# Kernel tuning notes

Measured on AMD Instinct MI355X. Metric: run time of the kernel, lower is better.

## Reference

```python
import jax, jax.numpy as jnp
import numpy as np
from jax import lax

# Config mirroring __init__ defaults
TEMP = 0.1           # temperature (constant schedule; set_epoch never called)
KSIZE = 11           # dilation_kernel_size
MAX_POS = 2048       # max_pos_per_image
NEG_RATIO = 5.0      # neg_pos_ratio
EPS = 1e-8
KN = int(NEG_RATIO * MAX_POS)   # max negatives per image (10240)
KC = 2 * KN                      # rim candidate pool for hard mining (20480)


def _forward(features, labels):
    B, C, H, W = features.shape
    HW = H * W
    fg = labels > 0                                   # (B,H,W)
    # Dilate foreground via max-pool (kernel KSIZE, stride 1, SAME) -> rim band
    dil = lax.reduce_window(fg.astype(jnp.float32), -jnp.inf, lax.max,
                            (1, KSIZE, KSIZE), (1, 1, 1), 'SAME') > 0
    rim = dil & (~fg)
    # L2-normalized per-pixel features, (B,HW,C)
    f = features.reshape(B, C, HW).transpose(0, 2, 1)
    f = f / jnp.maximum(jnp.linalg.norm(f, axis=-1, keepdims=True), EPS)
    fg_flat = fg.reshape(B, HW)
    rim_flat = rim.reshape(B, HW)
    rank = jnp.arange(HW, dtype=jnp.float32) / HW     # deterministic tiebreak

    def per_image(fi, fgi, rimi):
        # --- sample positives (deterministic raster-order selection of fg pixels) ---
        _, pidx = lax.top_k(fgi.astype(jnp.float32) * 2.0 - rank, MAX_POS)
        vp = fgi[pidx]                                # valid-positive mask (P,)
        pf = fi[pidx]                                 # (P,C)
        # --- rim candidate pool ---
        _, cidx = lax.top_k(rimi.astype(jnp.float32) * 2.0 - rank, KC)
        vc = rimi[cidx]
        cf = fi[cidx]                                 # (KC,C)
        # --- hard negative mining: negatives most similar to any positive ---
        sim = pf @ cf.T                               # (P,KC)
        max_sim = jnp.max(jnp.where(vp[:, None], sim, -jnp.inf), axis=0)
        nvals, nsel = lax.top_k(jnp.where(vc, max_sim, -jnp.inf), KN)
        n_allowed = jnp.minimum(jnp.floor(NEG_RATIO * jnp.sum(vp)), KN)
        vn = jnp.isfinite(nvals) & (jnp.arange(KN) < n_allowed)
        nf = cf[nsel]                                 # (KN,C)
        # --- contrastive loss: positives attract, rim negatives repel ---
        lpp = (pf @ pf.T) / TEMP                      # (P,P)
        lpn = (pf @ nf.T) / TEMP                      # (P,KN)
        eye = jnp.eye(MAX_POS, dtype=bool)
        mpp = vp[:, None] & vp[None, :] & (~eye)
        mpn = vp[:, None] & vn[None, :]
        NEGC = jnp.float32(-1e30)
        all_logits = jnp.concatenate([jnp.where(mpp, lpp, NEGC),
                                      jnp.where(mpn, lpn, NEGC)], axis=1)
        denom = jax.nn.logsumexp(all_logits, axis=1)  # (P,)
        npairs = jnp.sum(mpp, axis=1)
        li = -jnp.sum(jnp.where(mpp, lpp - denom[:, None], 0.0), axis=1) \
             / jnp.maximum(npairs, 1)
        av = vp & (npairs > 0)
        img_loss = jnp.sum(jnp.where(av, li, 0.0)) / jnp.maximum(jnp.sum(av), 1)
        return img_loss, jnp.any(av)

    losses, has = jax.vmap(per_image)(f, fg_flat, rim_flat)
    return jnp.sum(jnp.where(has, losses, 0.0)) / jnp.maximum(jnp.sum(has), 1)


def setup_inputs() -> dict:
    key = jax.random.key(0)
    k1, k2 = jax.random.split(key)
    features = jax.random.normal(k1, (4, 64, 384, 384), dtype=jnp.float32)
    labels = jax.random.randint(k2, (4, 384, 384), 0, 2).astype(jnp.int64)
    return {"features": features, "labels": labels}


def reference(features, labels):
    return _forward(features, labels)
```

## Files before the change

### kernel.cpp

```cpp
#include <hip/hip_runtime.h>
#include <hip/hip_bf16.h>

#define DEVI __device__ __forceinline__

static constexpr int cB = 4, cC = 64, cH = 384, cW = 384;
static constexpr int cHW = cH * cW;
static constexpr int cP  = 2048;
static constexpr int cKC = 20480;
static constexpr int cKN = 10240;
static constexpr int cNT = cP + cKN;
static constexpr float cTEMP_INV = 10.0f;
static constexpr int cCHUNK = 2048;
static constexpr int cNB = cHW / cCHUNK;
static constexpr int cNCH = 8;
static constexpr int cTPC = (cNT / 16) / cNCH;

using f32x4  = __attribute__((ext_vector_type(4))) float;
using bf16x8 = __attribute__((ext_vector_type(8))) __bf16;

static constexpr size_t off_fg   = 0;
static constexpr size_t off_tmp  = off_fg   + (size_t)cB * cHW;
static constexpr size_t off_rim  = off_tmp  + (size_t)cB * cHW;
static constexpr size_t off_pidx = off_rim  + (size_t)cB * cHW;
static constexpr size_t off_cidx = off_pidx + (size_t)cB * cP * 4;
static constexpr size_t off_scal = off_cidx + (size_t)cB * cKC * 4;
static constexpr size_t off_EL   = off_scal + 256;
static constexpr size_t off_msim = off_EL   + (size_t)cB * cP * 8;
static constexpr size_t off_nsel = off_msim + (size_t)cB * 2 * cKC * 4;
static constexpr size_t off_G    = off_nsel + (size_t)cB * cKN * 4;
static constexpr size_t off_cf   = off_G    + (size_t)cB * cNT * cC * 2;
static constexpr size_t off_bcnt = off_cf   + (size_t)cB * cKC * cC * 2;
static constexpr size_t off_boff = off_bcnt + (size_t)cB * cNB * 4;

__global__ void k_fg(const int* labels, unsigned char* fg) {
  int i = blockIdx.x * 256 + threadIdx.x;
  if (i < cB * cHW) fg[i] = labels[i] > 0;
}

__global__ void k_hdil(const unsigned char* fg, unsigned char* tmp) {
  int i = blockIdx.x * 256 + threadIdx.x;
  if (i >= cB * cHW) return;
  int x = i % cW;
  int rowbase = i - x;
  int lo = max(x - 5, 0), hi = min(x + 5, cW - 1);
  unsigned char m = 0;
  for (int xx = lo; xx <= hi; xx++) m |= fg[rowbase + xx];
  tmp[i] = m;
}

__global__ __launch_bounds__(256) void k_vdil_count(const unsigned char* tmp, const unsigned char* fg,
                                                    unsigned char* rim, int* blkcnt) {
  __shared__ int red[256];
  int b = blockIdx.y, blk = blockIdx.x, tid = threadIdx.x;
  int base = blk * cCHUNK + tid * 8;
  const unsigned char* tb  = tmp + (size_t)b * cHW;
  const unsigned char* fgb = fg  + (size_t)b * cHW;
  unsigned long long fv = *(const unsigned long long*)(fgb + base);
  unsigned long long pk = 0;
  int crim = 0;
#pragma unroll
  for (int e = 0; e < 8; e++) {
    int p = base + e;
    int y = p / cW, x = p - y * cW;
    int lo = max(y - 5, 0), hi = min(y + 5, cH - 1);
    unsigned char m = 0;
    for (int yy = lo; yy <= hi; yy++) m |= tb[yy * cW + x];
    unsigned char f = (unsigned char)((fv >> (8 * e)) & 1);
    unsigned char rv = m & (f ^ 1);
    pk |= (unsigned long long)rv << (8 * e);
    crim += rv;
  }
  *(unsigned long long*)(rim + (size_t)b * cHW + base) = pk;
  int cfg = __popcll(fv & 0x0101010101010101ULL);
  red[tid] = cfg | (crim << 16);
  __syncthreads();
  for (int s = 128; s > 0; s >>= 1) {
    if (tid < s) red[tid] += red[tid + s];
    __syncthreads();
  }
  if (tid == 0) blkcnt[b * cNB + blk] = red[0];
}

__global__ __launch_bounds__(128) void k_offsets(const int* blkcnt, int2* blkoff, int* scal) {
  __shared__ int sf[128], sr[128];
  int b = blockIdx.x, tid = threadIdx.x;
  int v = (tid < cNB) ? blkcnt[b * cNB + tid] : 0;
  int f = v & 0xffff, r = v >> 16;
  sf[tid] = f; sr[tid] = r;
  __syncthreads();
  for (int d = 1; d < 128; d <<= 1) {
    int tf = (tid >= d) ? sf[tid - d] : 0;
    int tr = (tid >= d) ? sr[tid - d] : 0;
    __syncthreads();
    sf[tid] += tf; sr[tid] += tr;
    __syncthreads();
  }
  if (tid < cNB) blkoff[b * cNB + tid] = make_int2(sf[tid] - f, sr[tid] - r);
  if (tid == 0) {
    int nfg = sf[cNB - 1], nrim = sr[cNB - 1];
    scal[b * 16 + 0] = nfg;
    scal[b * 16 + 1] = min(nfg, cP);
    scal[b * 16 + 2] = min(nrim, cKC);
    scal[b * 16 + 4] = nrim;
  }
}

__device__ int scan_excl_256(int v, int* lds) {
  int tid = threadIdx.x;
  lds[tid] = v;
  __syncthreads();
  for (int d = 1; d < 256; d <<= 1) {
    int t = (tid >= d) ? lds[tid - d] : 0;
    __syncthreads();
    lds[tid] += t;
    __syncthreads();
  }
  int e = lds[tid] - v;
  __syncthreads();
  return e;
}

__global__ __launch_bounds__(256) void k_scatter(const unsigned char* fg, const unsigned char* rim,
                                                 const int2* blkoff, const int* scal,
                                                 int* pidx, int* cidx) {
  __shared__ int lds[256];
  int b = blockIdx.y, blk = blockIdx.x, tid = threadIdx.x;
  int2 off = blkoff[b * cNB + blk];
  int nfg  = scal[b * 16 + 0];
  int nrim = scal[b * 16 + 4];
  bool needf = (off.x < cP)  || (nfg  < cP);
  bool needr = (off.y < cKC) || (nrim < cKC);
  if (!needf && !needr) return;
  int base = blk * cCHUNK + tid * 8;
  const unsigned char* fgb  = fg  + (size_t)b * cHW;
  const unsigned char* rimb = rim + (size_t)b * cHW;
  unsigned long long fv = *(const unsigned long long*)(fgb + base);
  unsigned long long rv = *(const unsigned long long*)(rimb + base);
  int cfg  = __popcll(fv & 0x0101010101010101ULL);
  int crim = __popcll(rv & 0x0101010101010101ULL);
  int ex = scan_excl_256(cfg | (crim << 16), lds);
  int of  = off.x + (ex & 0xffff);
  int orr = off.y + (ex >> 16);
  int* pout = pidx + (size_t)b * cP;
  int* cout = cidx + (size_t)b * cKC;
#pragma unroll
  for (int e = 0; e < 8; e++) {
    int p = base + e;
    int f = (int)((fv >> (8 * e)) & 1);
    int r = (int)((rv >> (8 * e)) & 1);
    if (f) { if (of < cP) pout[of] = p; of++; }
    else if (nfg < cP) { int o = nfg + (p - of); if (o < cP) pout[o] = p; }
    if (r) { if (orr < cKC) cout[orr] = p; orr++; }
    else if (nrim < cKC) { int o = nrim + (p - orr); if (o < cKC) cout[o] = p; }
  }
}

__global__ __launch_bounds__(256) void k_gather_norm(const float* feat, const int* idxs, int idx_stride,
                                                     int count, __hip_bfloat16* dst, size_t dst_img_stride) {
  int b = blockIdx.y;
  int i = blockIdx.x * 256 + threadIdx.x;
  if (i >= count) return;
  int p = idxs[(size_t)b * idx_stride + i];
  const float* fb = feat + (size_t)b * cC * cHW + p;
  float v[cC];
  float ss = 0.f;
#pragma unroll
  for (int c = 0; c < cC; c++) { float t = fb[(size_t)c * cHW]; v[c] = t; ss += t * t; }
  float sc = 1.0f / fmaxf(sqrtf(ss), 1e-8f);
  __hip_bfloat16* out = dst + (size_t)b * dst_img_stride + (size_t)i * cC;
#pragma unroll
  for (int c = 0; c < cC; c++) out[c] = __float2bfloat16(v[c] * sc);
}

__global__ __launch_bounds__(256) void k_mine(const __hip_bfloat16* G, const __hip_bfloat16* cf,
                                              const int* scal, float* msim) {
  int b = blockIdx.z, rc = blockIdx.y;
  int P_valid = scal[b * 16 + 1];
  int wave = threadIdx.x >> 6, lane = threadIdx.x & 63;
  int lr = lane & 15, quad = lane >> 4;
  int colbase = blockIdx.x * 128 + wave * 32;
  float* msout = msim + ((size_t)b * 2 + rc) * cKC;
  int mt0 = rc * (cP / 32);
  int chunk_lo = mt0 * 16;
  if (chunk_lo >= P_valid) {
    if (quad == 0) {
      msout[colbase + lr]      = -INFINITY;
      msout[colbase + 16 + lr] = -INFINITY;
    }
    return;
  }
  bool chunk_full = (chunk_lo + cP / 2) <= P_valid;
  const __bf16* pf  = (const __bf16*)(G  + (size_t)b * cNT * cC);
  const __bf16* cfb = (const __bf16*)(cf + (size_t)b * cKC * cC);

  bf16x8 bfr[2][2];
#pragma unroll
  for (int t = 0; t < 2; t++) {
    const __bf16* src = cfb + (size_t)(colbase + t * 16 + lr) * cC + quad * 8;
    bfr[t][0] = *(const bf16x8*)src;
    bfr[t][1] = *(const bf16x8*)(src + 32);
  }
  float cmax0 = -INFINITY, cmax1 = -INFINITY;
#pragma unroll 2
  for (int mt = mt0; mt < mt0 + cP / 32; mt++) {
    const __bf16* asrc = pf + (size_t)(mt * 16 + lr) * cC + quad * 8;
    bf16x8 a0 = *(const bf16x8*)asrc;
    bf16x8 a1 = *(const bf16x8*)(asrc + 32);
    f32x4 acc0 = {0, 0, 0, 0}, acc1 = {0, 0, 0, 0};
    acc0 = __builtin_amdgcn_mfma_f32_16x16x32_bf16(a0, bfr[0][0], acc0, 0, 0, 0);
    acc0 = __builtin_amdgcn_mfma_f32_16x16x32_bf16(a1, bfr[0][1], acc0, 0, 0, 0);
    acc1 = __builtin_amdgcn_mfma_f32_16x16x32_bf16(a0, bfr[1][0], acc1, 0, 0, 0);
    acc1 = __builtin_amdgcn_mfma_f32_16x16x32_bf16(a1, bfr[1][1], acc1, 0, 0, 0);
    if (chunk_full) {
#pragma unroll
      for (int r = 0; r < 4; r++) {
        cmax0 = fmaxf(cmax0, acc0[r]);
        cmax1 = fmaxf(cmax1, acc1[r]);
      }
    } else {
      int rb = mt * 16 + quad * 4;
#pragma unroll
      for (int r = 0; r < 4; r++) {
        bool rv = (rb + r) < P_valid;
        cmax0 = fmaxf(cmax0, rv ? acc0[r] : -INFINITY);
        cmax1 = fmaxf(cmax1, rv ? acc1[r] : -INFINITY);
      }
    }
  }
  cmax0 = fmaxf(cmax0, __shfl_xor(cmax0, 16));
  cmax0 = fmaxf(cmax0, __shfl_xor(cmax0, 32));
  cmax1 = fmaxf(cmax1, __shfl_xor(cmax1, 16));
  cmax1 = fmaxf(cmax1, __shfl_xor(cmax1, 32));
  if (quad == 0) {
    msout[colbase + lr]      = cmax0;
    msout[colbase + 16 + lr] = cmax1;
  }
}

DEVI unsigned f2key(float f) {
  unsigned u = __float_as_uint(f);
  return (u & 0x80000000u) ? ~u : (u | 0x80000000u);
}

__device__ int scan_excl_1024(int v, int* lds, int* total) {
  int tid = threadIdx.x;
  lds[tid] = v;
  __syncthreads();
  for (int d = 1; d < 1024; d <<= 1) {
    int t = (tid >= d) ? lds[tid - d] : 0;
    __syncthreads();
    lds[tid] += t;
    __syncthreads();
  }
  *total = lds[1023];
  int e = lds[tid] - v;
  __syncthreads();
  return e;
}

__global__ __launch_bounds__(1024) void k_selneg(const float* msim, int* nsel, int* scal) {
  __shared__ int hist[256];
  __shared__ int suf[256];
  __shared__ int lds[1024];
  __shared__ unsigned sh_prefix;
  __shared__ int sh_rem;
  int b = blockIdx.x, tid = threadIdx.x;
  const float* ms0 = msim + ((size_t)b * 2 + 0) * cKC;
  const float* ms1 = msim + ((size_t)b * 2 + 1) * cKC;
  int P_valid = scal[b * 16 + 1], C_valid = scal[b * 16 + 2];
  int n_allowed = min(5 * P_valid, cKN);
  int nfin = (P_valid > 0) ? C_valid : 0;
  int KEEP = min(n_allowed, nfin);
  if (tid == 0) scal[b * 16 + 3] = KEEP;
  if (KEEP == 0) return;

  unsigned prefix = 0;
  int remaining = KEEP;
  for (int shift = 24; shift >= 0; shift -= 8) {
    if (tid < 256) hist[tid] = 0;
    __syncthreads();
    for (int c = tid; c < cKC; c += 1024) {
      unsigned key = (c < C_valid) ? f2key(fmaxf(ms0[c], ms1[c])) : 0u;
      if (shift == 24 || (key >> (shift + 8)) == prefix)
        atomicAdd(&hist[(key >> shift) & 255], 1);
    }
    __syncthreads();
    if (tid < 256) suf[tid] = hist[tid];
    __syncthreads();
    for (int d = 1; d < 256; d <<= 1) {
      int t = (tid < 256 && tid + d < 256) ? suf[tid + d] : 0;
      __syncthreads();
      if (tid < 256) suf[tid] += t;
      __syncthreads();
    }
    if (tid < 256) {
      int s = suf[tid];
      int sn = (tid < 255) ? suf[tid + 1] : 0;
      if (s >= remaining && sn < remaining) {
        sh_prefix = (prefix << 8) | (unsigned)tid;
        sh_rem = remaining - sn;
      }
    }
    __syncthreads();
    prefix = sh_prefix; remaining = sh_rem;
    __syncthreads();
  }
  unsigned T = prefix;

  const int CH2 = cKC / 1024;
  int s = tid * CH2;
  unsigned keys[CH2];
  int cntA = 0, cntT = 0;
  for (int e = 0; e < CH2; e++) {
    int c = s + e;
    unsigned key = (c < C_valid) ? f2key(fmaxf(ms0[c], ms1[c])) : 0u;
    keys[e] = key;
    cntA += (key > T);
    cntT += (key == T);
  }
  int totA, totT;
  int offA = scan_excl_1024(cntA, lds, &totA);
  int offT = scan_excl_1024(cntT, lds, &totT);
  int* out = nsel + (size_t)b * cKN;
  int oa = offA, ot = offT;
  for (int e = 0; e < CH2; e++) {
    unsigned key = keys[e];
    if (key > T) { out[oa++] = s + e; }
    else if (key == T) { if (ot < remaining) out[totA + ot] = s + e; ot++; }
  }
}

__global__ __launch_bounds__(256) void k_gather_neg(const __hip_bfloat16* cf, const int* nsel,
                                                    const int* scal, __hip_bfloat16* G) {
  int b = blockIdx.y;
  int KEEP = scal[b * 16 + 3];
  int t = blockIdx.x * 256 + threadIdx.x;
  int k = t >> 3, part = t & 7;
  if (k >= cKN) return;
  int4 val = {0, 0, 0, 0};
  if (k < KEEP) {
    int src = nsel[(size_t)b * cKN + k];
    val = *(const int4*)((const __bf16*)(cf + (size_t)b * cKC * cC) + (size_t)src * cC + part * 8);
  }
  *(int4*)((__bf16*)(G + (size_t)b * cNT * cC) + (size_t)(cP + k) * cC + part * 8) = val;
}

__global__ __launch_bounds__(256) void k_loss_part(const __hip_bfloat16* G, const int* scal, float2* EL) {
  __shared__ float sE[4][32];
  __shared__ float sL[4][32];
  int b = blockIdx.z;
  int P_valid = scal[b * 16 + 1];
  int KEEP = scal[b * 16 + 3];
  int wave = threadIdx.x >> 6, lane = threadIdx.x & 63;
  int lr = lane & 15, quad = lane >> 4;
  int rowbase = blockIdx.x * 32;
  const __bf16* Gb = (const __bf16*)G + (size_t)b * cNT * cC;

  bf16x8 afr[2][2];
#pragma unroll
  for (int rt = 0; rt < 2; rt++) {
    const __bf16* src = Gb + (size_t)(rowbase + rt * 16 + lr) * cC + quad * 8;
    afr[rt][0] = *(const bf16x8*)src;
    afr[rt][1] = *(const bf16x8*)(src + 32);
  }
  float eacc[2][4] = {{0, 0, 0, 0}, {0, 0, 0, 0}};
  float lacc[2][4] = {{0, 0, 0, 0}, {0, 0, 0, 0}};
  int ct0 = blockIdx.y * cTPC;
  for (int ct = ct0 + wave; ct < ct0 + cTPC; ct += 4) {
    int tb = ct * 16;
    bool is_pos = tb < cP;
    int vlimit = is_pos ? P_valid : (cP + KEEP);
    if (tb >= vlimit) continue;
    bool all_valid = (tb + 16) <= vlimit;
    bool has_diag = is_pos && (tb >= rowbase) && (tb < rowbase + 32);
    const __bf16* bsrc = Gb + (size_t)(tb + lr) * cC + quad * 8;
    bf16x8 b0 = *(const bf16x8*)bsrc;
    bf16x8 b1 = *(const bf16x8*)(bsrc + 32);
    f32x4 acc[2];
#pragma unroll
    for (int rt = 0; rt < 2; rt++) {
      f32x4 a = {0, 0, 0, 0};
      a = __builtin_amdgcn_mfma_f32_16x16x32_bf16(afr[rt][0], b0, a, 0, 0, 0);
      a = __builtin_amdgcn_mfma_f32_16x16x32_bf16(afr[rt][1], b1, a, 0, 0, 0);
      acc[rt] = a;
    }
    if (all_valid && !has_diag) {
      if (is_pos) {
#pragma unroll
        for (int rt = 0; rt < 2; rt++)
#pragma unroll
          for (int r = 0; r < 4; r++) {
            float logit = acc[rt][r] * cTEMP_INV;
            eacc[rt][r] += __expf(logit);
            lacc[rt][r] += logit;
          }
      } else {
#pragma unroll
        for (int rt = 0; rt < 2; rt++)
#pragma unroll
          for (int r = 0; r < 4; r++)
            eacc[rt][r] += __expf(acc[rt][r] * cTEMP_INV);
      }
    } else {
      bool colv = (tb + lr) < vlimit;
#pragma unroll
      for (int rt = 0; rt < 2; rt++) {
        int rb = rowbase + rt * 16 + quad * 4;
#pragma unroll
        for (int r = 0; r < 4; r++) {
          float logit = acc[rt][r] * cTEMP_INV;
          bool use = colv && !(has_diag && (tb + lr) == (rb + r));
          float e = __expf(logit);
          eacc[rt][r] += use ? e : 0.0f;
          if (is_pos) lacc[rt][r] += use ? logit : 0.0f;
        }
      }
    }
  }
#pragma unroll
  for (int rt = 0; rt < 2; rt++) {
#pragma unroll
    for (int r = 0; r < 4; r++) {
      float e = eacc[rt][r], l = lacc[rt][r];
#pragma unroll
      for (int d = 1; d < 16; d <<= 1) {
        e += __shfl_xor(e, d);
        l += __shfl_xor(l, d);
      }
      if (lr == 0) {
        sE[wave][rt * 16 + quad * 4 + r] = e;
        sL[wave][rt * 16 + quad * 4 + r] = l;
      }
    }
  }
  __syncthreads();
  if (threadIdx.x < 32) {
    int row = rowbase + threadIdx.x;
    float E = sE[0][threadIdx.x] + sE[1][threadIdx.x] + sE[2][threadIdx.x] + sE[3][threadIdx.x];
    float L = sL[0][threadIdx.x] + sL[1][threadIdx.x] + sL[2][threadIdx.x] + sL[3][threadIdx.x];
    atomicAdd(&EL[(size_t)b * cP + row].x, E);
    atomicAdd(&EL[(size_t)b * cP + row].y, L);
  }
}

__global__ __launch_bounds__(1024) void k_loss_fin(const int* scal, const float2* EL, float* out) {
  __shared__ float ssum[16];
  int tid = threadIdx.x;
  int b = tid >> 8, t = tid & 255;
  int Pv = scal[b * 16 + 1];
  float s = 0.f;
  if (Pv >= 2) {
    float inv = 1.0f / (float)(Pv - 1);
#pragma unroll
    for (int e = 0; e < 8; e++) {
      int row = t * 8 + e;
      if (row < Pv) {
        float2 el = EL[(size_t)b * cP + row];
        s += logf(el.x) - el.y * inv;
      }
    }
  }
#pragma unroll
  for (int d = 1; d < 64; d <<= 1) s += __shfl_xor(s, d);
  if ((tid & 63) == 0) ssum[tid >> 6] = s;
  __syncthreads();
  if (tid == 0) {
    float tot = 0.f;
    int cnt = 0;
    for (int bb = 0; bb < cB; bb++) {
      int P = scal[bb * 16 + 1];
      if (P >= 2) {
        float is = ssum[bb * 4] + ssum[bb * 4 + 1] + ssum[bb * 4 + 2] + ssum[bb * 4 + 3];
        tot += is / (float)P;
        cnt++;
      }
    }
    out[0] = tot / (float)(cnt > 0 ? cnt : 1);
  }
}

extern "C" void kernel_launch(void* const* d_in, const int* in_sizes, int n_in,
                              void* d_out, int out_size, void* d_ws, size_t ws_size,
                              hipStream_t stream) {
  const float* feat = (const float*)d_in[0];
  const int* labels = (const int*)d_in[1];
  char* ws = (char*)d_ws;
  unsigned char* fg  = (unsigned char*)(ws + off_fg);
  unsigned char* tmp = (unsigned char*)(ws + off_tmp);
  unsigned char* rim = (unsigned char*)(ws + off_rim);
  int* pidx = (int*)(ws + off_pidx);
  int* cidx = (int*)(ws + off_cidx);
  int* scal = (int*)(ws + off_scal);
  float2* EL = (float2*)(ws + off_EL);
  float* msim = (float*)(ws + off_msim);
  int* nsel = (int*)(ws + off_nsel);
  __hip_bfloat16* G  = (__hip_bfloat16*)(ws + off_G);
  __hip_bfloat16* cf = (__hip_bfloat16*)(ws + off_cf);
  int* blkcnt = (int*)(ws + off_bcnt);
  int2* blkoff = (int2*)(ws + off_boff);
  float* out = (float*)d_out;

  int nElem = cB * cHW;
  hipMemsetAsync(EL, 0, (size_t)cB * cP * 8, stream);
  k_fg<<<(nElem + 255) / 256, 256, 0, stream>>>(labels, fg);
  k_hdil<<<(nElem + 255) / 256, 256, 0, stream>>>(fg, tmp);
  k_vdil_count<<<dim3(cNB, cB), 256, 0, stream>>>(tmp, fg, rim, blkcnt);
  k_offsets<<<cB, 128, 0, stream>>>(blkcnt, blkoff, scal);
  k_scatter<<<dim3(cNB, cB), 256, 0, stream>>>(fg, rim, blkoff, scal, pidx, cidx);
  k_gather_norm<<<dim3(cP / 256, cB), 256, 0, stream>>>(feat, pidx, cP, cP, G, (size_t)cNT * cC);
  k_gather_norm<<<dim3(cKC / 256, cB), 256, 0, stream>>>(feat, cidx, cKC, cKC, cf, (size_t)cKC * cC);
  k_mine<<<dim3(cKC / 128, 2, cB), 256, 0, stream>>>(G, cf, scal, msim);
  k_selneg<<<cB, 1024, 0, stream>>>(msim, nsel, scal);
  k_gather_neg<<<dim3(cKN * 8 / 256, cB), 256, 0, stream>>>(cf, nsel, scal, G);
  k_loss_part<<<dim3(cP / 32, cNCH, cB), 256, 0, stream>>>(G, scal, EL);
  k_loss_fin<<<1, 1024, 0, stream>>>(scal, EL, out);
}
```

Baseline: 416.9 us.

## Fuse preprocessing kernels, widen mining and loss tiles, drop atomics

Merges the fg threshold and horizontal dilation into one bit-packed kernel and vectorizes the vertical dilation over 8-byte words. Merges the two gather-normalize launches into one. Widens k_mine to 128 columns per wave with A-fragment prefetch, and k_loss_part to 64 rows per block. Per-chunk partial sums replace atomics and the memset, and the final kernel reduces them. These cut launch count, redundant loads and atomic traffic, at the cost of more register pressure and fewer blocks in the mining and loss kernels.

```diff
diff --git a/kernel.cpp b/kernel.cpp
--- a/kernel.cpp
+++ b/kernel.cpp
@@ -25,27 +25,37 @@
 static constexpr size_t off_cidx = off_pidx + (size_t)cB * cP * 4;
 static constexpr size_t off_scal = off_cidx + (size_t)cB * cKC * 4;
 static constexpr size_t off_EL   = off_scal + 256;
-static constexpr size_t off_msim = off_EL   + (size_t)cB * cP * 8;
+static constexpr size_t off_msim = off_EL   + (size_t)cNCH * cB * cP * 8;
 static constexpr size_t off_nsel = off_msim + (size_t)cB * 2 * cKC * 4;
 static constexpr size_t off_G    = off_nsel + (size_t)cB * cKN * 4;
 static constexpr size_t off_cf   = off_G    + (size_t)cB * cNT * cC * 2;
 static constexpr size_t off_bcnt = off_cf   + (size_t)cB * cKC * cC * 2;
 static constexpr size_t off_boff = off_bcnt + (size_t)cB * cNB * 4;
 
-__global__ void k_fg(const int* labels, unsigned char* fg) {
-  int i = blockIdx.x * 256 + threadIdx.x;
-  if (i < cB * cHW) fg[i] = labels[i] > 0;
-}
-
-__global__ void k_hdil(const unsigned char* fg, unsigned char* tmp) {
-  int i = blockIdx.x * 256 + threadIdx.x;
-  if (i >= cB * cHW) return;
-  int x = i % cW;
-  int rowbase = i - x;
-  int lo = max(x - 5, 0), hi = min(x + 5, cW - 1);
-  unsigned char m = 0;
-  for (int xx = lo; xx <= hi; xx++) m |= fg[rowbase + xx];
-  tmp[i] = m;
+DEVI f32x4 mfma16(bf16x8 a, bf16x8 b, f32x4 c) {
+  return __builtin_amdgcn_mfma_f32_16x16x32_bf16(a, b, c, 0, 0, 0);
+}
+
+__global__ __launch_bounds__(256) void k_fg_hdil(const int* labels, unsigned char* fg, unsigned char* tmp) {
+  int t = blockIdx.x * 256 + threadIdx.x;
+  int base = t * 8;
+  int x0 = base % cW;
+  const int* lb = labels + (base - x0);
+  unsigned m = 0;
+#pragma unroll
+  for (int j = 0; j < 18; j++) {
+    int x = x0 - 5 + j;
+    int v = (x >= 0 && x < cW) ? (lb[x] > 0) : 0;
+    m |= (unsigned)v << j;
+  }
+  unsigned long long fgb = 0, tmb = 0;
+#pragma unroll
+  for (int e = 0; e < 8; e++) {
+    fgb |= (unsigned long long)((m >> (e + 5)) & 1u) << (8 * e);
+    tmb |= (unsigned long long)(((m >> e) & 0x7FFu) ? 1u : 0u) << (8 * e);
+  }
+  *(unsigned long long*)(fg + base)  = fgb;
+  *(unsigned long long*)(tmp + base) = tmb;
 }
 
 __global__ __launch_bounds__(256) void k_vdil_count(const unsigned char* tmp, const unsigned char* fg,
@@ -56,22 +66,14 @@
   const unsigned char* tb  = tmp + (size_t)b * cHW;
   const unsigned char* fgb = fg  + (size_t)b * cHW;
   unsigned long long fv = *(const unsigned long long*)(fgb + base);
-  unsigned long long pk = 0;
-  int crim = 0;
-#pragma unroll
-  for (int e = 0; e < 8; e++) {
-    int p = base + e;
-    int y = p / cW, x = p - y * cW;
-    int lo = max(y - 5, 0), hi = min(y + 5, cH - 1);
-    unsigned char m = 0;
-    for (int yy = lo; yy <= hi; yy++) m |= tb[yy * cW + x];
-    unsigned char f = (unsigned char)((fv >> (8 * e)) & 1);
-    unsigned char rv = m & (f ^ 1);
-    pk |= (unsigned long long)rv << (8 * e);
-    crim += rv;
-  }
+  int y = base / cW, x = base % cW;
+  int lo = max(y - 5, 0), hi = min(y + 5, cH - 1);
+  unsigned long long m8 = 0;
+  for (int yy = lo; yy <= hi; yy++) m8 |= *(const unsigned long long*)(tb + yy * cW + x);
+  unsigned long long pk = m8 & (fv ^ 0x0101010101010101ULL);
   *(unsigned long long*)(rim + (size_t)b * cHW + base) = pk;
-  int cfg = __popcll(fv & 0x0101010101010101ULL);
+  int cfg  = __popcll(fv & 0x0101010101010101ULL);
+  int crim = __popcll(pk & 0x0101010101010101ULL);
   red[tid] = cfg | (crim << 16);
   __syncthreads();
   for (int s = 128; s > 0; s >>= 1) {
@@ -155,19 +157,27 @@
   }
 }
 
-__global__ __launch_bounds__(256) void k_gather_norm(const float* feat, const int* idxs, int idx_stride,
-                                                     int count, __hip_bfloat16* dst, size_t dst_img_stride) {
+__global__ __launch_bounds__(256) void k_gather_norm(const float* feat, const int* pidx, const int* cidx,
+                                                     __hip_bfloat16* G, __hip_bfloat16* cf) {
   int b = blockIdx.y;
-  int i = blockIdx.x * 256 + threadIdx.x;
-  if (i >= count) return;
-  int p = idxs[(size_t)b * idx_stride + i];
+  int bx = blockIdx.x;
+  int p;
+  __hip_bfloat16* out;
+  if (bx < cP / 256) {
+    int i = bx * 256 + threadIdx.x;
+    p = pidx[(size_t)b * cP + i];
+    out = G + (size_t)b * cNT * cC + (size_t)i * cC;
+  } else {
+    int i = (bx - cP / 256) * 256 + threadIdx.x;
+    p = cidx[(size_t)b * cKC + i];
+    out = cf + (size_t)b * cKC * cC + (size_t)i * cC;
+  }
   const float* fb = feat + (size_t)b * cC * cHW + p;
   float v[cC];
   float ss = 0.f;
 #pragma unroll
   for (int c = 0; c < cC; c++) { float t = fb[(size_t)c * cHW]; v[c] = t; ss += t * t; }
   float sc = 1.0f / fmaxf(sqrtf(ss), 1e-8f);
-  __hip_bfloat16* out = dst + (size_t)b * dst_img_stride + (size_t)i * cC;
 #pragma unroll
   for (int c = 0; c < cC; c++) out[c] = __float2bfloat16(v[c] * sc);
 }
@@ -178,62 +188,66 @@
   int P_valid = scal[b * 16 + 1];
   int wave = threadIdx.x >> 6, lane = threadIdx.x & 63;
   int lr = lane & 15, quad = lane >> 4;
-  int colbase = blockIdx.x * 128 + wave * 32;
+  int colbase = (blockIdx.x * 4 + wave) * 128;
   float* msout = msim + ((size_t)b * 2 + rc) * cKC;
-  int mt0 = rc * (cP / 32);
+  int mt0 = rc * 64;
   int chunk_lo = mt0 * 16;
   if (chunk_lo >= P_valid) {
     if (quad == 0) {
-      msout[colbase + lr]      = -INFINITY;
-      msout[colbase + 16 + lr] = -INFINITY;
+#pragma unroll
+      for (int tt = 0; tt < 8; tt++) msout[colbase + tt * 16 + lr] = -INFINITY;
     }
     return;
   }
-  bool chunk_full = (chunk_lo + cP / 2) <= P_valid;
+  bool chunk_full = (chunk_lo + 1024) <= P_valid;
   const __bf16* pf  = (const __bf16*)(G  + (size_t)b * cNT * cC);
   const __bf16* cfb = (const __bf16*)(cf + (size_t)b * cKC * cC);
 
-  bf16x8 bfr[2][2];
-#pragma unroll
-  for (int t = 0; t < 2; t++) {
-    const __bf16* src = cfb + (size_t)(colbase + t * 16 + lr) * cC + quad * 8;
-    bfr[t][0] = *(const bf16x8*)src;
-    bfr[t][1] = *(const bf16x8*)(src + 32);
-  }
-  float cmax0 = -INFINITY, cmax1 = -INFINITY;
-#pragma unroll 2
-  for (int mt = mt0; mt < mt0 + cP / 32; mt++) {
-    const __bf16* asrc = pf + (size_t)(mt * 16 + lr) * cC + quad * 8;
-    bf16x8 a0 = *(const bf16x8*)asrc;
-    bf16x8 a1 = *(const bf16x8*)(asrc + 32);
-    f32x4 acc0 = {0, 0, 0, 0}, acc1 = {0, 0, 0, 0};
-    acc0 = __builtin_amdgcn_mfma_f32_16x16x32_bf16(a0, bfr[0][0], acc0, 0, 0, 0);
-    acc0 = __builtin_amdgcn_mfma_f32_16x16x32_bf16(a1, bfr[0][1], acc0, 0, 0, 0);
-    acc1 = __builtin_amdgcn_mfma_f32_16x16x32_bf16(a0, bfr[1][0], acc1, 0, 0, 0);
-    acc1 = __builtin_amdgcn_mfma_f32_16x16x32_bf16(a1, bfr[1][1], acc1, 0, 0, 0);
-    if (chunk_full) {
-#pragma unroll
-      for (int r = 0; r < 4; r++) {
-        cmax0 = fmaxf(cmax0, acc0[r]);
-        cmax1 = fmaxf(cmax1, acc1[r]);
-      }
-    } else {
-      int rb = mt * 16 + quad * 4;
-#pragma unroll
-      for (int r = 0; r < 4; r++) {
-        bool rv = (rb + r) < P_valid;
-        cmax0 = fmaxf(cmax0, rv ? acc0[r] : -INFINITY);
-        cmax1 = fmaxf(cmax1, rv ? acc1[r] : -INFINITY);
-      }
-    }
-  }
-  cmax0 = fmaxf(cmax0, __shfl_xor(cmax0, 16));
-  cmax0 = fmaxf(cmax0, __shfl_xor(cmax0, 32));
-  cmax1 = fmaxf(cmax1, __shfl_xor(cmax1, 16));
-  cmax1 = fmaxf(cmax1, __shfl_xor(cmax1, 32));
+  bf16x8 bfr[8][2];
+#pragma unroll
+  for (int tt = 0; tt < 8; tt++) {
+    const __bf16* src = cfb + (size_t)(colbase + tt * 16 + lr) * cC + quad * 8;
+    bfr[tt][0] = *(const bf16x8*)src;
+    bfr[tt][1] = *(const bf16x8*)(src + 32);
+  }
+  float cmax[8];
+#pragma unroll
+  for (int tt = 0; tt < 8; tt++) cmax[tt] = -INFINITY;
+
+  const __bf16* ap = pf + (size_t)(mt0 * 16 + lr) * cC + quad * 8;
+  bf16x8 a0 = *(const bf16x8*)ap;
+  bf16x8 a1 = *(const bf16x8*)(ap + 32);
+  for (int mt = mt0; mt < mt0 + 64; mt++) {
+    int nmt = min(mt + 1, mt0 + 63);
+    const __bf16* np = pf + (size_t)(nmt * 16 + lr) * cC + quad * 8;
+    bf16x8 na0 = *(const bf16x8*)np;
+    bf16x8 na1 = *(const bf16x8*)(np + 32);
+    int rb = mt * 16 + quad * 4;
+#pragma unroll
+    for (int tt = 0; tt < 8; tt++) {
+      f32x4 acc = {0, 0, 0, 0};
+      acc = mfma16(a0, bfr[tt][0], acc);
+      acc = mfma16(a1, bfr[tt][1], acc);
+      if (chunk_full) {
+        cmax[tt] = fmaxf(cmax[tt], fmaxf(fmaxf(acc[0], acc[1]), fmaxf(acc[2], acc[3])));
+      } else {
+#pragma unroll
+        for (int r = 0; r < 4; r++)
+          cmax[tt] = fmaxf(cmax[tt], (rb + r) < P_valid ? acc[r] : -INFINITY);
+      }
+    }
+    a0 = na0; a1 = na1;
+  }
+#pragma unroll
+  for (int tt = 0; tt < 8; tt++) {
+    float c = cmax[tt];
+    c = fmaxf(c, __shfl_xor(c, 16));
+    c = fmaxf(c, __shfl_xor(c, 32));
+    cmax[tt] = c;
+  }
   if (quad == 0) {
-    msout[colbase + lr]      = cmax0;
-    msout[colbase + 16 + lr] = cmax1;
+#pragma unroll
+    for (int tt = 0; tt < 8; tt++) msout[colbase + tt * 16 + lr] = cmax[tt];
   }
 }
 
@@ -345,49 +359,50 @@
   *(int4*)((__bf16*)(G + (size_t)b * cNT * cC) + (size_t)(cP + k) * cC + part * 8) = val;
 }
 
-__global__ __launch_bounds__(256) void k_loss_part(const __hip_bfloat16* G, const int* scal, float2* EL) {
-  __shared__ float sE[4][32];
-  __shared__ float sL[4][32];
-  int b = blockIdx.z;
+__global__ __launch_bounds__(256) void k_loss_part(const __hip_bfloat16* G, const int* scal, float2* ELp) {
+  __shared__ float sE[4][64];
+  __shared__ float sL[4][64];
+  int b = blockIdx.z, chunk = blockIdx.y;
   int P_valid = scal[b * 16 + 1];
   int KEEP = scal[b * 16 + 3];
+  if (P_valid < 2) return;
   int wave = threadIdx.x >> 6, lane = threadIdx.x & 63;
   int lr = lane & 15, quad = lane >> 4;
-  int rowbase = blockIdx.x * 32;
+  int rowbase = blockIdx.x * 64;
   const __bf16* Gb = (const __bf16*)G + (size_t)b * cNT * cC;
 
-  bf16x8 afr[2][2];
-#pragma unroll
-  for (int rt = 0; rt < 2; rt++) {
+  bf16x8 afr[4][2];
+#pragma unroll
+  for (int rt = 0; rt < 4; rt++) {
     const __bf16* src = Gb + (size_t)(rowbase + rt * 16 + lr) * cC + quad * 8;
     afr[rt][0] = *(const bf16x8*)src;
     afr[rt][1] = *(const bf16x8*)(src + 32);
   }
-  float eacc[2][4] = {{0, 0, 0, 0}, {0, 0, 0, 0}};
-  float lacc[2][4] = {{0, 0, 0, 0}, {0, 0, 0, 0}};
-  int ct0 = blockIdx.y * cTPC;
+  float eacc[4][4] = {};
+  float lacc[4][4] = {};
+  int ct0 = chunk * cTPC;
   for (int ct = ct0 + wave; ct < ct0 + cTPC; ct += 4) {
     int tb = ct * 16;
     bool is_pos = tb < cP;
     int vlimit = is_pos ? P_valid : (cP + KEEP);
     if (tb >= vlimit) continue;
     bool all_valid = (tb + 16) <= vlimit;
-    bool has_diag = is_pos && (tb >= rowbase) && (tb < rowbase + 32);
+    bool has_diag = is_pos && (tb >= rowbase) && (tb < rowbase + 64);
     const __bf16* bsrc = Gb + (size_t)(tb + lr) * cC + quad * 8;
     bf16x8 b0 = *(const bf16x8*)bsrc;
     bf16x8 b1 = *(const bf16x8*)(bsrc + 32);
-    f32x4 acc[2];
-#pragma unroll
-    for (int rt = 0; rt < 2; rt++) {
+    f32x4 acc[4];
+#pragma unroll
+    for (int rt = 0; rt < 4; rt++) {
       f32x4 a = {0, 0, 0, 0};
-      a = __builtin_amdgcn_mfma_f32_16x16x32_bf16(afr[rt][0], b0, a, 0, 0, 0);
-      a = __builtin_amdgcn_mfma_f32_16x16x32_bf16(afr[rt][1], b1, a, 0, 0, 0);
+      a = mfma16(afr[rt][0], b0, a);
+      a = mfma16(afr[rt][1], b1, a);
       acc[rt] = a;
     }
     if (all_valid && !has_diag) {
       if (is_pos) {
 #pragma unroll
-        for (int rt = 0; rt < 2; rt++)
+        for (int rt = 0; rt < 4; rt++)
 #pragma unroll
           for (int r = 0; r < 4; r++) {
             float logit = acc[rt][r] * cTEMP_INV;
@@ -396,7 +411,7 @@
           }
       } else {
 #pragma unroll
-        for (int rt = 0; rt < 2; rt++)
+        for (int rt = 0; rt < 4; rt++)
 #pragma unroll
           for (int r = 0; r < 4; r++)
             eacc[rt][r] += __expf(acc[rt][r] * cTEMP_INV);
@@ -404,7 +419,7 @@
     } else {
       bool colv = (tb + lr) < vlimit;
 #pragma unroll
-      for (int rt = 0; rt < 2; rt++) {
+      for (int rt = 0; rt < 4; rt++) {
         int rb = rowbase + rt * 16 + quad * 4;
 #pragma unroll
         for (int r = 0; r < 4; r++) {
@@ -418,7 +433,7 @@
     }
   }
 #pragma unroll
-  for (int rt = 0; rt < 2; rt++) {
+  for (int rt = 0; rt < 4; rt++) {
 #pragma unroll
     for (int r = 0; r < 4; r++) {
       float e = eacc[rt][r], l = lacc[rt][r];
@@ -434,16 +449,15 @@
     }
   }
   __syncthreads();
-  if (threadIdx.x < 32) {
+  if (threadIdx.x < 64) {
     int row = rowbase + threadIdx.x;
     float E = sE[0][threadIdx.x] + sE[1][threadIdx.x] + sE[2][threadIdx.x] + sE[3][threadIdx.x];
     float L = sL[0][threadIdx.x] + sL[1][threadIdx.x] + sL[2][threadIdx.x] + sL[3][threadIdx.x];
-    atomicAdd(&EL[(size_t)b * cP + row].x, E);
-    atomicAdd(&EL[(size_t)b * cP + row].y, L);
-  }
-}
-
-__global__ __launch_bounds__(1024) void k_loss_fin(const int* scal, const float2* EL, float* out) {
+    ELp[((size_t)chunk * cB + b) * cP + row] = make_float2(E, L);
+  }
+}
+
+__global__ __launch_bounds__(1024) void k_loss_fin(const int* scal, const float2* ELp, float* out) {
   __shared__ float ssum[16];
   int tid = threadIdx.x;
   int b = tid >> 8, t = tid & 255;
@@ -455,8 +469,13 @@
     for (int e = 0; e < 8; e++) {
       int row = t * 8 + e;
       if (row < Pv) {
-        float2 el = EL[(size_t)b * cP + row];
-        s += logf(el.x) - el.y * inv;
+        float E = 0.f, L = 0.f;
+#pragma unroll
+        for (int ch = 0; ch < cNCH; ch++) {
+          float2 el = ELp[((size_t)ch * cB + b) * cP + row];
+          E += el.x; L += el.y;
+        }
+        s += logf(E) - L * inv;
       }
     }
   }
@@ -491,7 +510,7 @@
   int* pidx = (int*)(ws + off_pidx);
   int* cidx = (int*)(ws + off_cidx);
   int* scal = (int*)(ws + off_scal);
-  float2* EL = (float2*)(ws + off_EL);
+  float2* ELp = (float2*)(ws + off_EL);
   float* msim = (float*)(ws + off_msim);
   int* nsel = (int*)(ws + off_nsel);
   __hip_bfloat16* G  = (__hip_bfloat16*)(ws + off_G);
@@ -500,18 +519,14 @@
   int2* blkoff = (int2*)(ws + off_boff);
   float* out = (float*)d_out;
 
-  int nElem = cB * cHW;
-  hipMemsetAsync(EL, 0, (size_t)cB * cP * 8, stream);
-  k_fg<<<(nElem + 255) / 256, 256, 0, stream>>>(labels, fg);
-  k_hdil<<<(nElem + 255) / 256, 256, 0, stream>>>(fg, tmp);
+  k_fg_hdil<<<cB * cHW / 8 / 256, 256, 0, stream>>>(labels, fg, tmp);
   k_vdil_count<<<dim3(cNB, cB), 256, 0, stream>>>(tmp, fg, rim, blkcnt);
   k_offsets<<<cB, 128, 0, stream>>>(blkcnt, blkoff, scal);
   k_scatter<<<dim3(cNB, cB), 256, 0, stream>>>(fg, rim, blkoff, scal, pidx, cidx);
-  k_gather_norm<<<dim3(cP / 256, cB), 256, 0, stream>>>(feat, pidx, cP, cP, G, (size_t)cNT * cC);
-  k_gather_norm<<<dim3(cKC / 256, cB), 256, 0, stream>>>(feat, cidx, cKC, cKC, cf, (size_t)cKC * cC);
-  k_mine<<<dim3(cKC / 128, 2, cB), 256, 0, stream>>>(G, cf, scal, msim);
+  k_gather_norm<<<dim3(cP / 256 + cKC / 256, cB), 256, 0, stream>>>(feat, pidx, cidx, G, cf);
+  k_mine<<<dim3(cKC / 512, 2, cB), 256, 0, stream>>>(G, cf, scal, msim);
   k_selneg<<<cB, 1024, 0, stream>>>(msim, nsel, scal);
   k_gather_neg<<<dim3(cKN * 8 / 256, cB), 256, 0, stream>>>(cf, nsel, scal, G);
-  k_loss_part<<<dim3(cP / 32, cNCH, cB), 256, 0, stream>>>(G, scal, EL);
-  k_loss_fin<<<1, 1024, 0, stream>>>(scal, EL, out);
-}
+  k_loss_part<<<dim3(cP / 64, cNCH, cB), 256, 0, stream>>>(G, scal, ELp);
+  k_loss_fin<<<1, 1024, 0, stream>>>(scal, ELp, out);
+}
```

New measurement: 370.0 us. -11.3%, faster.
